# Optimization experiments

Measured on AMD Instinct MI355X. Metric: run time of the kernel, lower is better.

## Reference

```python
import jax, jax.numpy as jnp
import numpy as np

S = 1024; VOCAB = 100000; EMB = 300
POS_SZ = 64; CHAR_E = 50; CHAR_ENC = 128; WLEN = 16
NCHARS = 100; NPOSTAG = 50; NPOSITIONS = 1024
D = EMB + 3 * POS_SZ + CHAR_ENC  # word_rep_size = 620
BIH = 128   # per-direction LSTM hidden (bilstm_hidden_size // 2)
TLH = 256; LCC = 128; GCC = 256
NET = 8; NTAGS = 16; NREL = 16
TOKF = 2 * BIH + LCC + TLH       # 640
SENTF = 2 * TOKF + GCC           # 1536

def _p(k, shape):
    return 0.02 * jax.random.normal(k, shape, dtype=jnp.float32)

def setup_inputs():
    key = jax.random.key(0)
    ks = jax.random.split(key, 30)
    return {
        'word_inputs': jax.random.randint(ks[0], (1, S), 0, VOCAB),
        'char_inputs': jax.random.randint(ks[1], (1, S, WLEN), 0, NCHARS),
        'postag_inputs': jax.random.randint(ks[2], (1, S), 0, NPOSTAG),
        'dependency_inputs': jax.random.randint(ks[3], (1, S), 0, 64),
        'position_inputs': jax.random.randint(ks[4], (1, S), 0, NPOSITIONS),
        'topo_order': jnp.arange(S),  # children-before-parents order
        'parent': jnp.concatenate([jnp.arange(1, S), jnp.array([S])]),  # chain dep tree; root -> dummy slot S
        'pointed_token_idx': 5,
        'word_table': _p(ks[5], (VOCAB, EMB)),
        'char_table': _p(ks[6], (NCHARS, CHAR_E)),
        'char_conv_w': _p(ks[7], (CHAR_ENC, CHAR_E, 3)),
        'char_conv_b': jnp.zeros((CHAR_ENC,), jnp.float32),
        'postag_table': _p(ks[8], (NPOSTAG, POS_SZ)),
        'position_table': _p(ks[9], (NPOSITIONS, POS_SZ)),
        'lstm_f_Wx': _p(ks[10], (D, 4 * BIH)),
        'lstm_f_Wh': _p(ks[11], (BIH, 4 * BIH)),
        'lstm_f_b': jnp.zeros((4 * BIH,), jnp.float32),
        'lstm_b_Wx': _p(ks[12], (D, 4 * BIH)),
        'lstm_b_Wh': _p(ks[13], (BIH, 4 * BIH)),
        'lstm_b_b': jnp.zeros((4 * BIH,), jnp.float32),
        'word_cnn_w': _p(ks[14], (LCC, D, 3)),
        'word_cnn_b': jnp.zeros((LCC,), jnp.float32),
        'tl_Wiou': _p(ks[15], (D, 3 * TLH)),
        'tl_Uiou': _p(ks[16], (TLH, 3 * TLH)),
        'tl_biou': jnp.zeros((3 * TLH,), jnp.float32),
        'tl_Wf': _p(ks[17], (D, TLH)),
        'tl_Uf': _p(ks[18], (TLH, TLH)),
        'tl_bf': jnp.zeros((TLH,), jnp.float32),
        'sent_cnn_w': _p(ks[19], (GCC, D, 3)),
        'sent_cnn_b': jnp.zeros((GCC,), jnp.float32),
        'et_w': _p(ks[20], (GCC + TOKF, NET)),
        'et_b': jnp.zeros((NET,), jnp.float32),
        'crf_w': _p(ks[21], (SENTF, NTAGS)),
        'crf_b': jnp.zeros((NTAGS,), jnp.float32),
        'crf_trans': _p(ks[22], (NTAGS, NTAGS)),
        'rel_w': _p(ks[23], (SENTF, NREL)),
        'rel_b': jnp.zeros((NREL,), jnp.float32),
    }

def _conv1d(x, w, b):
    # x: [N, Cin, W], w: [Cout, Cin, K], padding=1 (matches nn.Conv1d(..., padding=1))
    y = jax.lax.conv_general_dilated(x, w, (1,), [(1, 1)], dimension_numbers=('NCW', 'OIW', 'NCW'))
    return y + b[None, :, None]

def _lstm(xs, Wx, Wh, b):
    H = Wh.shape[0]
    def step(carry, x):
        h, c = carry
        g = x @ Wx + h @ Wh + b
        i, f, gg, o = jnp.split(g, 4, axis=-1)
        c = jax.nn.sigmoid(f) * c + jax.nn.sigmoid(i) * jnp.tanh(gg)
        h = jax.nn.sigmoid(o) * jnp.tanh(c)
        return (h, c), h
    init = (jnp.zeros((H,), xs.dtype), jnp.zeros((H,), xs.dtype))
    _, hs = jax.lax.scan(step, init, xs)
    return hs

def _tree_lstm(x, order, parent, Wiou, Uiou, biou, Wf, Uf, bf):
    # ChildSum TreeLSTM over the whole dependency tree in topological order.
    # Equivalent to the source's per-token subtree recursion: each node's h
    # only depends on its subtree.
    Sn, H = x.shape[0], Uf.shape[0]
    xiou = x @ Wiou + biou                 # [S, 3H]
    xf = jnp.concatenate([x @ Wf + bf, jnp.zeros((1, H), x.dtype)], axis=0)  # dummy row for root's parent
    def step(carry, j):
        h, hsum, fcsum = carry
        iou = xiou[j] + hsum[j] @ Uiou
        i, o, u = jnp.split(iou, 3)
        cj = jax.nn.sigmoid(i) * jnp.tanh(u) + fcsum[j]
        hj = jax.nn.sigmoid(o) * jnp.tanh(cj)
        p = parent[j]
        f = jax.nn.sigmoid(xf[p] + hj @ Uf)  # per-child forget gate
        return (h.at[j].set(hj), hsum.at[p].add(hj), fcsum.at[p].add(f * cj)), None
    h0 = jnp.zeros((Sn, H), x.dtype)
    acc0 = jnp.zeros((Sn + 1, H), x.dtype)
    (h, _, _), _ = jax.lax.scan(step, (h0, acc0, acc0), order)
    return h

def _viterbi(emissions, trans):
    # emissions: [S, T]; trans[i, j] = score(i -> j)
    def step(score, e):
        s = score[:, None] + trans
        return jnp.max(s, axis=0) + e, jnp.argmax(s, axis=0)
    final, ptrs = jax.lax.scan(step, emissions[0], emissions[1:])
    last = jnp.argmax(final)
    def bt(tag, p):
        prev = p[tag]
        return prev, prev
    _, prevs = jax.lax.scan(bt, last, ptrs, reverse=True)
    return jnp.concatenate([prevs, last[None]])

def reference(word_inputs, char_inputs, postag_inputs, dependency_inputs, position_inputs, topo_order, parent, pointed_token_idx, word_table, char_table, char_conv_w, char_conv_b, postag_table, position_table, lstm_f_Wx, lstm_f_Wh, lstm_f_b, lstm_b_Wx, lstm_b_Wh, lstm_b_b, word_cnn_w, word_cnn_b, tl_Wiou, tl_Uiou, tl_biou, tl_Wf, tl_Uf, tl_bf, sent_cnn_w, sent_cnn_b, et_w, et_b, crf_w, crf_b, crf_trans, rel_w, rel_b):
    we = word_table[word_inputs]                                   # [1,S,EMB]
    cx = jnp.transpose(char_table[char_inputs[0]], (0, 2, 1))      # [S,CHAR_E,WLEN]
    ce = jnp.max(jax.nn.relu(_conv1d(cx, char_conv_w, char_conv_b)), axis=-1)[None]  # CharCNN -> [1,S,CHAR_ENC]
    pe = postag_table[postag_inputs]
    poe = position_table[position_inputs]
    de = position_table[dependency_inputs]                         # faithful to source bug: uses position table
    inputs = jnp.concatenate([we, ce, pe, poe, de], axis=-1)       # [1,S,D]
    x = inputs[0]
    hf = _lstm(x, lstm_f_Wx, lstm_f_Wh, lstm_f_b)
    hb = _lstm(x[::-1], lstm_b_Wx, lstm_b_Wh, lstm_b_b)[::-1]
    bilstm = jnp.concatenate([hf, hb], axis=-1)[None]              # [1,S,2*BIH]
    xc = jnp.transpose(inputs, (0, 2, 1))                          # [1,D,S]
    local_cnn = jnp.transpose(_conv1d(xc, word_cnn_w, word_cnn_b), (0, 2, 1))
    tree_h = _tree_lstm(x, topo_order, parent, tl_Wiou, tl_Uiou, tl_biou, tl_Wf, tl_Uf, tl_bf)[None]
    global_cnn = jnp.transpose(jnp.max(_conv1d(xc, sent_cnn_w, sent_cnn_b), axis=-1, keepdims=True), (0, 2, 1))  # [1,1,GCC]
    tokens_info = jnp.concatenate([bilstm, local_cnn, tree_h], axis=-1)  # [1,S,TOKF]
    ptr = tokens_info[:, pointed_token_idx, :]                     # [1,TOKF]
    ptr_info = jnp.broadcast_to(ptr[:, None, :], (1, S, TOKF))
    glob_info = jnp.broadcast_to(global_cnn, (1, S, GCC))
    sentence_encoding = jnp.concatenate([tokens_info, ptr_info, glob_info], axis=-1)  # dropout = identity (eval)
    one_vec = jnp.concatenate([global_cnn[:, 0, :], ptr], axis=-1)
    entitytype = jax.nn.softmax(one_vec @ et_w + et_b, axis=-1)
    entities = _viterbi(sentence_encoding[0] @ crf_w + crf_b, crf_trans)
    relations = jax.nn.sigmoid(sentence_encoding @ rel_w + rel_b)
    return sentence_encoding, entitytype, entities, relations
```

## Files before the change

### kernel.cpp

```cpp
#include <hip/hip_runtime.h>
#include <math.h>

#define SEQ   1024
#define DX    620
#define BIH   128
#define TLH   256
#define NTAGS 16

#define O_X      0
#define O_XGF    634880
#define O_XGB    (O_XGF + 524288)
#define O_XIOU   (O_XGB + 524288)
#define O_XF     (O_XIOU + 786432)
#define O_LCNN   (O_XF + 262400)
#define O_SCNN   (O_LCNN + 131072)
#define O_PART   (O_SCNN + 262144)
#define O_GCNN   (O_PART + 4096)
#define O_HF     (O_GCNN + 256)
#define O_HB     (O_HF + 131072)
#define O_TREEH  (O_HB + 131072)
#define O_IOUA   (O_TREEH + 262144)
#define O_FCSUM  (O_IOUA + 787200)
#define O_EMIS   (O_FCSUM + 262400)
#define O_CNT    (O_EMIS + 16384)

#define SENT 0xFFFFFFFFu

__device__ __forceinline__ float sig_f(float x){ return 1.0f/(1.0f + __expf(-x)); }
__device__ __forceinline__ float tanh_f(float x){
  float ax = fabsf(x);
  float e  = __expf(-2.0f*ax);
  float t  = (1.0f - e)/(1.0f + e);
  return x < 0.0f ? -t : t;
}

__global__ __launch_bounds__(128) void k_embed(
    const int* __restrict__ wi, const int* __restrict__ ci,
    const int* __restrict__ postag_in, const int* __restrict__ dep_in, const int* __restrict__ pos_in,
    const float* __restrict__ word_table, const float* __restrict__ char_table,
    const float* __restrict__ ccw, const float* __restrict__ ccb,
    const float* __restrict__ postag_table, const float* __restrict__ position_table,
    float* __restrict__ x)
{
  int s = blockIdx.x;
  int tid = threadIdx.x;
  __shared__ __align__(16) float ce[50][16];
  for (int idx = tid; idx < 800; idx += 128){
    int e = idx >> 4, t = idx & 15;
    ce[e][t] = char_table[ci[s*16 + t]*50 + e];
  }
  __syncthreads();
  float* xr = x + (size_t)s*DX;
  const float* wrow = word_table + (size_t)wi[s]*300;
  for (int d = tid; d < 300; d += 128) xr[d] = wrow[d];
  {
    int oc = tid;
    const float* wp = ccw + oc*150;
    float acc[16];
    float b = ccb[oc];
    #pragma unroll
    for (int t=0;t<16;t++) acc[t] = b;
    for (int ic=0; ic<50; ic++){
      float w0 = wp[ic*3+0], w1 = wp[ic*3+1], w2 = wp[ic*3+2];
      float cv[16];
      float4 c0 = *(const float4*)&ce[ic][0];
      float4 c1 = *(const float4*)&ce[ic][4];
      float4 c2 = *(const float4*)&ce[ic][8];
      float4 c3 = *(const float4*)&ce[ic][12];
      cv[0]=c0.x;cv[1]=c0.y;cv[2]=c0.z;cv[3]=c0.w;
      cv[4]=c1.x;cv[5]=c1.y;cv[6]=c1.z;cv[7]=c1.w;
      cv[8]=c2.x;cv[9]=c2.y;cv[10]=c2.z;cv[11]=c2.w;
      cv[12]=c3.x;cv[13]=c3.y;cv[14]=c3.z;cv[15]=c3.w;
      #pragma unroll
      for (int t=0;t<16;t++){
        float a = cv[t]*w1;
        if (t > 0)  a += cv[t-1]*w0;
        if (t < 15) a += cv[t+1]*w2;
        acc[t] += a;
      }
    }
    float m = acc[0];
    #pragma unroll
    for (int t=1;t<16;t++) m = fmaxf(m, acc[t]);
    xr[300 + oc] = fmaxf(m, 0.0f);
  }
  if (tid < 64){
    int d = tid;
    xr[428 + d] = postag_table[postag_in[s]*64 + d];
    xr[492 + d] = position_table[pos_in[s]*64 + d];
    xr[556 + d] = position_table[dep_in[s]*64 + d];
  }
}

struct GemmArgs {
  const float* B[6];
  const float* bias[6];
  float*       C[6];
  int N[6]; int K[6]; int amode[6];
};

__global__ __launch_bounds__(256) void k_gemm(const float* __restrict__ x, GemmArgs ga)
{
  int z = blockIdx.z;
  int N = ga.N[z], K = ga.K[z], amode = ga.amode[z];
  int bn = blockIdx.x*64;
  if (bn >= N) return;
  int bm = blockIdx.y*64;
  const float* __restrict__ Bm = ga.B[z];
  __shared__ __align__(16) float As[20][64];
  __shared__ __align__(16) float Bs[20][64];
  int tid = threadIdx.x;
  int lane = tid & 63, kg = tid >> 6;
  int tx = tid & 15, ty = tid >> 4;
  float acc[4][4] = {{0.f}};
  for (int k0 = 0; k0 < K; k0 += 20){
    #pragma unroll
    for (int kk=0; kk<5; kk++){
      int k = kg*5 + kk;
      float av;
      if (amode == 0){
        av = x[(size_t)(bm+lane)*DX + k0 + k];
      } else {
        int kc = k0 + k;
        int d  = kc/3;
        int sh = kc - d*3 - 1;
        int row = bm + lane + sh;
        av = (row >= 0 && row < SEQ) ? x[(size_t)row*DX + d] : 0.0f;
      }
      As[k][lane] = av;
      Bs[k][lane] = (amode==0) ? Bm[(size_t)(k0+k)*N + bn + lane]
                               : Bm[(size_t)(bn+lane)*K + k0 + k];
    }
    __syncthreads();
    #pragma unroll
    for (int k=0;k<20;k++){
      float4 a = *(const float4*)&As[k][ty<<2];
      float4 b = *(const float4*)&Bs[k][tx<<2];
      acc[0][0]+=a.x*b.x; acc[0][1]+=a.x*b.y; acc[0][2]+=a.x*b.z; acc[0][3]+=a.x*b.w;
      acc[1][0]+=a.y*b.x; acc[1][1]+=a.y*b.y; acc[1][2]+=a.y*b.z; acc[1][3]+=a.y*b.w;
      acc[2][0]+=a.z*b.x; acc[2][1]+=a.z*b.y; acc[2][2]+=a.z*b.z; acc[2][3]+=a.z*b.w;
      acc[3][0]+=a.w*b.x; acc[3][1]+=a.w*b.y; acc[3][2]+=a.w*b.z; acc[3][3]+=a.w*b.w;
    }
    __syncthreads();
  }
  const float* bias = ga.bias[z];
  float* C = ga.C[z];
  float4 bb;
  bb.x = bias[bn+(tx<<2)+0]; bb.y = bias[bn+(tx<<2)+1];
  bb.z = bias[bn+(tx<<2)+2]; bb.w = bias[bn+(tx<<2)+3];
  #pragma unroll
  for (int i=0;i<4;i++){
    int row = bm + (ty<<2) + i;
    float4 o;
    o.x = acc[i][0] + bb.x; o.y = acc[i][1] + bb.y;
    o.z = acc[i][2] + bb.z; o.w = acc[i][3] + bb.w;
    *(float4*)&C[(size_t)row*N + bn + (tx<<2)] = o;
  }
}

__global__ __launch_bounds__(256) void k_gmax(const float* __restrict__ scnn, float* __restrict__ gcnn){
  int c = threadIdx.x;
  float m = -3.0e38f;
  #pragma unroll 8
  for (int s = 0; s < SEQ; s++) m = fmaxf(m, scnn[(size_t)s*256 + c]);
  gcnn[c] = m;
}

__global__ __launch_bounds__(1024) void k_recur(
    const float* __restrict__ xg_f, const float* __restrict__ xg_b,
    const float* __restrict__ Wh_f, const float* __restrict__ Wh_b,
    const float* __restrict__ xiou, const float* __restrict__ xf,
    const float* __restrict__ Uiou, const float* __restrict__ Uf,
    const int* __restrict__ order, const int* __restrict__ parent,
    float* __restrict__ hf, float* __restrict__ hb,
    float* tree_h, float* iou_acc, float* fcsum)
{
  int blk = blockIdx.x;
  int tid = threadIdx.x;

  if (blk >= 4){
    const float* xg  = (blk == 4) ? xg_f : xg_b;
    const float* Wh  = (blk == 4) ? Wh_f : Wh_b;
    float* hout      = (blk == 4) ? hf : hb;
    int col = tid & 511, half = tid >> 9;
    float4 w4[16];
    #pragma unroll
    for (int r=0;r<16;r++){
      w4[r].x = Wh[(size_t)(half*64 + r*4+0)*512 + col];
      w4[r].y = Wh[(size_t)(half*64 + r*4+1)*512 + col];
      w4[r].z = Wh[(size_t)(half*64 + r*4+2)*512 + col];
      w4[r].w = Wh[(size_t)(half*64 + r*4+3)*512 + col];
    }
    __shared__ __align__(16) float lhl[BIH];
    __shared__ float lcst[BIH];
    __shared__ float pr[512];
    __shared__ float gl[512];
    if (tid < BIH){ lhl[tid] = 0.f; lcst[tid] = 0.f; }
    __syncthreads();
    for (int st=0; st<SEQ; st++){
      int n = (blk == 4) ? st : (SEQ-1-st);
      float xgv = (half == 0) ? xg[(size_t)n*512 + col] : 0.f;
      float a = 0.f;
      #pragma unroll
      for (int r=0;r<16;r++){
        float4 h4 = *(const float4*)&lhl[half*64 + r*4];
        a += h4.x*w4[r].x + h4.y*w4[r].y + h4.z*w4[r].z + h4.w*w4[r].w;
      }
      if (half) pr[col] = a;
      __syncthreads();
      if (!half) gl[col] = a + pr[col] + xgv;
      __syncthreads();
      if (tid < BIH){
        float gi = gl[tid], gf = gl[BIH+tid], gg = gl[2*BIH+tid], go = gl[3*BIH+tid];
        float c = sig_f(gf)*lcst[tid] + sig_f(gi)*tanh_f(gg);
        float h = sig_f(go)*tanh_f(c);
        lcst[tid] = c;
        lhl[tid] = h;
        hout[(size_t)n*BIH + tid] = h;
      }
      __syncthreads();
    }
    return;
  }

  int q = tid >> 8;
  int c = tid & 255;
  float4 w4[16];
  if (c < 192){
    int gcol = (c>>6)*TLH + blk*64 + (c&63);
    #pragma unroll
    for (int r=0;r<16;r++){
      w4[r].x = Uiou[(size_t)(q*64 + r*4+0)*768 + gcol];
      w4[r].y = Uiou[(size_t)(q*64 + r*4+1)*768 + gcol];
      w4[r].z = Uiou[(size_t)(q*64 + r*4+2)*768 + gcol];
      w4[r].w = Uiou[(size_t)(q*64 + r*4+3)*768 + gcol];
    }
  } else {
    int fcol = blk*64 + (c-192);
    #pragma unroll
    for (int r=0;r<16;r++){
      w4[r].x = Uf[(size_t)(q*64 + r*4+0)*256 + fcol];
      w4[r].y = Uf[(size_t)(q*64 + r*4+1)*256 + fcol];
      w4[r].z = Uf[(size_t)(q*64 + r*4+2)*256 + fcol];
      w4[r].w = Uf[(size_t)(q*64 + r*4+3)*256 + fcol];
    }
  }
  __shared__ __align__(16) float hl[TLH];
  __shared__ float part[256][5];
  __shared__ float cprev[64];
  __shared__ float passv[256];
  __shared__ int ord_l[SEQ];
  __shared__ int par_l[SEQ];
  for (int i=tid; i<SEQ; i+=1024){ ord_l[i] = order[i]; par_l[i] = parent[i]; }
  int ulo = blk*64, uhi = blk*64 + 64;
  __syncthreads();

  for (int t=0; t<SEQ; t++){
    int n = ord_l[t];
    bool ppeq = false;
    float xi=0.f, xo=0.f, xu=0.f;
    if (tid < 64){
      int u = ulo + tid;
      xi = xiou[(size_t)n*768 + u];
      xo = xiou[(size_t)n*768 + 256 + u];
      xu = xiou[(size_t)n*768 + 512 + u];
    }
    if (t > 0){
      int m  = ord_l[t-1];
      int pp = par_l[m];
      ppeq = (pp == n);
      float oldv = 0.f, xfv = 0.f;
      if (tid < 192){
        oldv = iou_acc[(size_t)pp*768 + (tid>>6)*TLH + ulo + (tid&63)];
      } else if (tid < 256){
        int fc = ulo + (tid-192);
        oldv = fcsum[(size_t)pp*256 + fc];
        xfv  = xf[(size_t)pp*256 + fc];
      }
      float a = 0.f;
      #pragma unroll
      for (int r=0;r<16;r++){
        float4 h4 = *(const float4*)&hl[q*64 + r*4];
        a += h4.x*w4[r].x + h4.y*w4[r].y + h4.z*w4[r].z + h4.w*w4[r].w;
      }
      part[c][q] = a;
      __syncthreads();
      if (tid < 256){
        float v = part[tid][0] + part[tid][1] + part[tid][2] + part[tid][3];
        if (tid < 192){
          float tot = oldv + v;
          iou_acc[(size_t)pp*768 + (tid>>6)*TLH + ulo + (tid&63)] = tot;
          passv[tid] = tot;
        } else {
          float fg = sig_f(xfv + v);
          float tot = oldv + fg * cprev[tid-192];
          fcsum[(size_t)pp*256 + ulo + (tid-192)] = tot;
          passv[tid] = tot;
        }
      }
      __syncthreads();
    }
    if (tid < 64){
      int u = ulo + tid;
      float ai, ao, au, fcs;
      if (ppeq){
        ai = passv[tid]; ao = passv[64+tid]; au = passv[128+tid]; fcs = passv[192+tid];
      } else {
        ai = iou_acc[(size_t)n*768 + u];
        ao = iou_acc[(size_t)n*768 + 256 + u];
        au = iou_acc[(size_t)n*768 + 512 + u];
        fcs = fcsum[(size_t)n*256 + u];
      }
      float cc = sig_f(xi + ai)*tanh_f(xu + au) + fcs;
      float hh = sig_f(xo + ao)*tanh_f(cc);
      cprev[tid] = cc;
      hl[u] = hh;
      __hip_atomic_store(&tree_h[(size_t)n*TLH + u], hh, __ATOMIC_RELAXED, __HIP_MEMORY_SCOPE_AGENT);
    }
    if (tid < 256 && (tid < ulo || tid >= uhi)){
      const unsigned* tp = (const unsigned*)(tree_h + (size_t)n*TLH + tid);
      unsigned v = __hip_atomic_load(tp, __ATOMIC_RELAXED, __HIP_MEMORY_SCOPE_AGENT);
      while (v == SENT){
        __builtin_amdgcn_s_sleep(1);
        v = __hip_atomic_load(tp, __ATOMIC_RELAXED, __HIP_MEMORY_SCOPE_AGENT);
      }
      hl[tid] = __uint_as_float(v);
    }
    __syncthreads();
  }
}

__global__ __launch_bounds__(256) void k_assemble(
    const float* __restrict__ hf, const float* __restrict__ hb,
    const float* __restrict__ lcnn, const float* __restrict__ tree_h,
    const float* __restrict__ gcnn,
    const float* __restrict__ crf_w, const float* __restrict__ crf_b,
    const float* __restrict__ rel_w, const float* __restrict__ rel_b,
    const int* __restrict__ ptk,
    float* __restrict__ se_out, float* __restrict__ emis, float* __restrict__ rel_out)
{
  int s = blockIdx.x, tid = threadIdx.x;
  int p = ptk[0];
  __shared__ float se[1536];
  for (int d = tid; d < 1536; d += 256){
    float v;
    if      (d < 128)  v = hf[(size_t)s*128 + d];
    else if (d < 256)  v = hb[(size_t)s*128 + d-128];
    else if (d < 384)  v = lcnn[(size_t)s*128 + d-256];
    else if (d < 640)  v = tree_h[(size_t)s*256 + d-384];
    else if (d < 768)  v = hf[(size_t)p*128 + d-640];
    else if (d < 896)  v = hb[(size_t)p*128 + d-768];
    else if (d < 1024) v = lcnn[(size_t)p*128 + d-896];
    else if (d < 1280) v = tree_h[(size_t)p*256 + d-1024];
    else               v = gcnn[d-1280];
    se[d] = v;
    se_out[(size_t)s*1536 + d] = v;
  }
  __syncthreads();
  int o = tid >> 3, l = tid & 7;
  const float* W = (o < 16) ? crf_w : rel_w;
  int oc = (o < 16) ? o : (o - 16);
  float a = 0.f;
  for (int k = l; k < 1536; k += 8) a += se[k]*W[(size_t)k*16 + oc];
  for (int off = 4; off; off >>= 1) a += __shfl_down(a, off, 8);
  if (l == 0){
    if (o < 16) emis[(size_t)s*16 + o] = a + crf_b[o];
    else        rel_out[(size_t)s*16 + oc] = sig_f(a + rel_b[oc]);
  }
}

__global__ __launch_bounds__(256) void k_entity(
    const float* __restrict__ hf, const float* __restrict__ hb,
    const float* __restrict__ lcnn, const float* __restrict__ tree_h,
    const float* __restrict__ gcnn,
    const float* __restrict__ et_w, const float* __restrict__ et_b,
    const int* __restrict__ ptk, float* __restrict__ out_et)
{
  __shared__ float ov[896];
  __shared__ float lg[8];
  int tid = threadIdx.x;
  int p = ptk[0];
  for (int d = tid; d < 896; d += 256){
    float v;
    if      (d < 256) v = gcnn[d];
    else if (d < 384) v = hf[(size_t)p*128 + d-256];
    else if (d < 512) v = hb[(size_t)p*128 + d-384];
    else if (d < 640) v = lcnn[(size_t)p*128 + d-512];
    else              v = tree_h[(size_t)p*256 + d-640];
    ov[d] = v;
  }
  __syncthreads();
  int o = tid >> 5, l = tid & 31;
  float a = 0.f;
  for (int k = l; k < 896; k += 32) a += ov[k]*et_w[(size_t)k*8 + o];
  for (int off = 16; off; off >>= 1) a += __shfl_down(a, off, 32);
  if (l == 0) lg[o] = a + et_b[o];
  __syncthreads();
  if (tid == 0){
    float mx = lg[0];
    for (int i=1;i<8;i++) mx = fmaxf(mx, lg[i]);
    float e[8], sum = 0.f;
    for (int i=0;i<8;i++){ e[i] = __expf(lg[i]-mx); sum += e[i]; }
    for (int i=0;i<8;i++) out_et[i] = e[i]/sum;
  }
}

__global__ __launch_bounds__(128) void k_viterbi(
    const float* __restrict__ emis, const float* __restrict__ trans, float* __restrict__ out_e)
{
  __shared__ float ring[64][16];
  __shared__ float sc[16], nsc[16];
  __shared__ float tr[256];
  __shared__ unsigned char ptrs[1023*16];
  int tid = threadIdx.x;
  for (int i=tid; i<256; i+=128) tr[i] = trans[i];
  for (int i=tid; i<33*16; i+=128) ring[i>>4][i&15] = emis[i];
  if (tid < 16) sc[tid] = emis[tid];
  __syncthreads();
  int j = (tid & 63) >> 2, iq = tid & 3;
  for (int t=1; t<1024; t++){
    if (tid >= 64){
      int lr = tid - 64;
      int tl = t + 32;
      if (lr < 16 && tl < 1024) ring[tl & 63][lr] = emis[(size_t)tl*16 + lr];
    } else {
      float best = -3.0e38f; int barg = 0;
      #pragma unroll
      for (int ii=0; ii<4; ii++){
        int i = iq*4 + ii;
        float v = sc[i] + tr[i*16 + j];
        if (v > best){ best = v; barg = i; }
      }
      #pragma unroll
      for (int off=1; off<4; off<<=1){
        float ovv = __shfl_down(best, off, 4);
        int   oaa = __shfl_down(barg, off, 4);
        if (ovv > best){ best = ovv; barg = oaa; }
      }
      if (iq == 0){
        nsc[j] = best + ring[t & 63][j];
        ptrs[(t-1)*16 + j] = (unsigned char)barg;
      }
    }
    __syncthreads();
    if (tid < 16) sc[tid] = nsc[tid];
    __syncthreads();
  }
  if (tid == 0){
    float b = sc[0]; int last = 0;
    #pragma unroll
    for (int i=1;i<16;i++){ if (sc[i] > b){ b = sc[i]; last = i; } }
    out_e[1023] = (float)last;
    int cur = last;
    for (int t=1022; t>=0; t--){ cur = (int)ptrs[t*16 + cur]; out_e[t] = (float)cur; }
  }
}

extern "C" void kernel_launch(void* const* d_in, const int* in_sizes, int n_in,
                              void* d_out, int out_size, void* d_ws, size_t ws_size,
                              hipStream_t stream)
{
  (void)in_sizes; (void)n_in; (void)out_size; (void)ws_size;
  const int*   wi         = (const int*)d_in[0];
  const int*   ci         = (const int*)d_in[1];
  const int*   postag_in  = (const int*)d_in[2];
  const int*   dep_in     = (const int*)d_in[3];
  const int*   pos_in     = (const int*)d_in[4];
  const int*   order      = (const int*)d_in[5];
  const int*   parent     = (const int*)d_in[6];
  const int*   ptk        = (const int*)d_in[7];
  const float* word_table = (const float*)d_in[8];
  const float* char_table = (const float*)d_in[9];
  const float* ccw        = (const float*)d_in[10];
  const float* ccb        = (const float*)d_in[11];
  const float* postag_tab = (const float*)d_in[12];
  const float* pos_tab    = (const float*)d_in[13];
  const float* Wx_f       = (const float*)d_in[14];
  const float* Wh_f       = (const float*)d_in[15];
  const float* b_f        = (const float*)d_in[16];
  const float* Wx_b       = (const float*)d_in[17];
  const float* Wh_b       = (const float*)d_in[18];
  const float* b_b        = (const float*)d_in[19];
  const float* wcnn_w     = (const float*)d_in[20];
  const float* wcnn_b     = (const float*)d_in[21];
  const float* Wiou       = (const float*)d_in[22];
  const float* Uiou       = (const float*)d_in[23];
  const float* biou       = (const float*)d_in[24];
  const float* Wf_t       = (const float*)d_in[25];
  const float* Uf_t       = (const float*)d_in[26];
  const float* bf_t       = (const float*)d_in[27];
  const float* scnn_w     = (const float*)d_in[28];
  const float* scnn_b     = (const float*)d_in[29];
  const float* et_w       = (const float*)d_in[30];
  const float* et_b       = (const float*)d_in[31];
  const float* crf_w      = (const float*)d_in[32];
  const float* crf_b      = (const float*)d_in[33];
  const float* crf_trans  = (const float*)d_in[34];
  const float* rel_w      = (const float*)d_in[35];
  const float* rel_b      = (const float*)d_in[36];

  float* ws = (float*)d_ws;
  float* x      = ws + O_X;
  float* xg_f   = ws + O_XGF;
  float* xg_b   = ws + O_XGB;
  float* xiou   = ws + O_XIOU;
  float* xf     = ws + O_XF;
  float* lcnn   = ws + O_LCNN;
  float* scnn   = ws + O_SCNN;
  float* gcnn   = ws + O_GCNN;
  float* hf     = ws + O_HF;
  float* hb     = ws + O_HB;
  float* tree_h = ws + O_TREEH;
  float* iou_acc= ws + O_IOUA;
  float* fcsum  = ws + O_FCSUM;
  float* emis   = ws + O_EMIS;

  float* outF     = (float*)d_out;
  float* se_out   = outF;
  float* et_out   = outF + 1572864;
  float* ent_out  = outF + 1572872;
  float* rel_out  = outF + 1573896;

  hipMemsetAsync(xf, 0, (size_t)1025*256*sizeof(float), stream);
  hipMemsetAsync(iou_acc, 0, ((size_t)1025*768 + 1025*256)*sizeof(float), stream);
  hipMemsetAsync(tree_h, 0xFF, (size_t)1024*256*sizeof(float), stream);

  k_embed<<<SEQ, 128, 0, stream>>>(wi, ci, postag_in, dep_in, pos_in,
                                   word_table, char_table, ccw, ccb,
                                   postag_tab, pos_tab, x);

  GemmArgs ga;
  ga.B[0]=Wx_f;  ga.bias[0]=b_f;   ga.C[0]=xg_f; ga.N[0]=512; ga.K[0]=620;  ga.amode[0]=0;
  ga.B[1]=Wx_b;  ga.bias[1]=b_b;   ga.C[1]=xg_b; ga.N[1]=512; ga.K[1]=620;  ga.amode[1]=0;
  ga.B[2]=Wiou;  ga.bias[2]=biou;  ga.C[2]=xiou; ga.N[2]=768; ga.K[2]=620;  ga.amode[2]=0;
  ga.B[3]=Wf_t;  ga.bias[3]=bf_t;  ga.C[3]=xf;   ga.N[3]=256; ga.K[3]=620;  ga.amode[3]=0;
  ga.B[4]=wcnn_w;ga.bias[4]=wcnn_b;ga.C[4]=lcnn; ga.N[4]=128; ga.K[4]=1860; ga.amode[4]=1;
  ga.B[5]=scnn_w;ga.bias[5]=scnn_b;ga.C[5]=scnn; ga.N[5]=256; ga.K[5]=1860; ga.amode[5]=1;
  k_gemm<<<dim3(12,16,6), 256, 0, stream>>>(x, ga);

  k_gmax<<<1, 256, 0, stream>>>(scnn, gcnn);

  k_recur<<<6, 1024, 0, stream>>>(xg_f, xg_b, Wh_f, Wh_b, xiou, xf, Uiou, Uf_t,
                                  order, parent, hf, hb, tree_h, iou_acc, fcsum);

  k_assemble<<<SEQ, 256, 0, stream>>>(hf, hb, lcnn, tree_h, gcnn,
                                      crf_w, crf_b, rel_w, rel_b, ptk,
                                      se_out, emis, rel_out);

  k_entity<<<1, 256, 0, stream>>>(hf, hb, lcnn, tree_h, gcnn, et_w, et_b, ptk, et_out);

  k_viterbi<<<1, 128, 0, stream>>>(emis, crf_trans, ent_out);
}
```

Before: 2.912 ms.

## Shrink recurrent blocks to 512 threads and cut per-step barriers

The recurrent kernel now runs 512 threads per block, each holding 128 weight rows in registers. The BiLSTM drops the two-half split, its shared partial-sum buffer and one barrier per step. The tree-LSTM splits each column across a thread pair, reduces with a lane shuffle, and moves the global loads of accumulator and parent state ahead of the matvec, which removes one barrier per step. Cross-block hidden-state polling now uses 48 threads reading four values each, without sleeping. In exchange, register pressure per thread roughly doubles, and the busy-wait spin without sleep may add memory contention.

```diff
diff --git a/kernel.cpp b/kernel.cpp
--- a/kernel.cpp
+++ b/kernel.cpp
@@ -22,7 +22,6 @@
 #define O_IOUA   (O_TREEH + 262144)
 #define O_FCSUM  (O_IOUA + 787200)
 #define O_EMIS   (O_FCSUM + 262400)
-#define O_CNT    (O_EMIS + 16384)
 
 #define SENT 0xFFFFFFFFu
 
@@ -166,7 +165,7 @@
   gcnn[c] = m;
 }
 
-__global__ __launch_bounds__(1024) void k_recur(
+__global__ __launch_bounds__(512, 2) void k_recur(
     const float* __restrict__ xg_f, const float* __restrict__ xg_b,
     const float* __restrict__ Wh_f, const float* __restrict__ Wh_b,
     const float* __restrict__ xiou, const float* __restrict__ xf,
@@ -182,33 +181,33 @@
     const float* xg  = (blk == 4) ? xg_f : xg_b;
     const float* Wh  = (blk == 4) ? Wh_f : Wh_b;
     float* hout      = (blk == 4) ? hf : hb;
-    int col = tid & 511, half = tid >> 9;
-    float4 w4[16];
-    #pragma unroll
-    for (int r=0;r<16;r++){
-      w4[r].x = Wh[(size_t)(half*64 + r*4+0)*512 + col];
-      w4[r].y = Wh[(size_t)(half*64 + r*4+1)*512 + col];
-      w4[r].z = Wh[(size_t)(half*64 + r*4+2)*512 + col];
-      w4[r].w = Wh[(size_t)(half*64 + r*4+3)*512 + col];
-    }
+    int col = tid;
+    float4 w4[32];
+    #pragma unroll
+    for (int r=0;r<32;r++){
+      w4[r].x = Wh[(size_t)(r*4+0)*512 + col];
+      w4[r].y = Wh[(size_t)(r*4+1)*512 + col];
+      w4[r].z = Wh[(size_t)(r*4+2)*512 + col];
+      w4[r].w = Wh[(size_t)(r*4+3)*512 + col];
+    }
+    #pragma unroll
+    for (int r=0;r<32;r++)
+      asm volatile("" : "+v"(w4[r].x), "+v"(w4[r].y), "+v"(w4[r].z), "+v"(w4[r].w));
     __shared__ __align__(16) float lhl[BIH];
     __shared__ float lcst[BIH];
-    __shared__ float pr[512];
     __shared__ float gl[512];
     if (tid < BIH){ lhl[tid] = 0.f; lcst[tid] = 0.f; }
     __syncthreads();
+    const float4* lhl4 = (const float4*)lhl;
     for (int st=0; st<SEQ; st++){
       int n = (blk == 4) ? st : (SEQ-1-st);
-      float xgv = (half == 0) ? xg[(size_t)n*512 + col] : 0.f;
-      float a = 0.f;
+      float a = xg[(size_t)n*512 + col];
       #pragma unroll
-      for (int r=0;r<16;r++){
-        float4 h4 = *(const float4*)&lhl[half*64 + r*4];
+      for (int r=0;r<32;r++){
+        float4 h4 = lhl4[r];
         a += h4.x*w4[r].x + h4.y*w4[r].y + h4.z*w4[r].z + h4.w*w4[r].w;
       }
-      if (half) pr[col] = a;
-      __syncthreads();
-      if (!half) gl[col] = a + pr[col] + xgv;
+      gl[col] = a;
       __syncthreads();
       if (tid < BIH){
         float gi = gl[tid], gf = gl[BIH+tid], gg = gl[2*BIH+tid], go = gl[3*BIH+tid];
@@ -223,108 +222,112 @@
     return;
   }
 
-  int q = tid >> 8;
-  int c = tid & 255;
-  float4 w4[16];
-  if (c < 192){
-    int gcol = (c>>6)*TLH + blk*64 + (c&63);
-    #pragma unroll
-    for (int r=0;r<16;r++){
-      w4[r].x = Uiou[(size_t)(q*64 + r*4+0)*768 + gcol];
-      w4[r].y = Uiou[(size_t)(q*64 + r*4+1)*768 + gcol];
-      w4[r].z = Uiou[(size_t)(q*64 + r*4+2)*768 + gcol];
-      w4[r].w = Uiou[(size_t)(q*64 + r*4+3)*768 + gcol];
-    }
-  } else {
-    int fcol = blk*64 + (c-192);
-    #pragma unroll
-    for (int r=0;r<16;r++){
-      w4[r].x = Uf[(size_t)(q*64 + r*4+0)*256 + fcol];
-      w4[r].y = Uf[(size_t)(q*64 + r*4+1)*256 + fcol];
-      w4[r].z = Uf[(size_t)(q*64 + r*4+2)*256 + fcol];
-      w4[r].w = Uf[(size_t)(q*64 + r*4+3)*256 + fcol];
-    }
-  }
+  int colh = tid >> 1, half = tid & 1;
+  int ulo = blk*64;
+  float4 w4[32];
+  {
+    const float* Wsrc; size_t stride; int gcol;
+    if (colh < 192){ Wsrc = Uiou; stride = 768; gcol = (colh>>6)*TLH + ulo + (colh&63); }
+    else           { Wsrc = Uf;   stride = 256; gcol = ulo + (colh-192); }
+    #pragma unroll
+    for (int r=0;r<32;r++){
+      int row = half*128 + r*4;
+      w4[r].x = Wsrc[(size_t)(row+0)*stride + gcol];
+      w4[r].y = Wsrc[(size_t)(row+1)*stride + gcol];
+      w4[r].z = Wsrc[(size_t)(row+2)*stride + gcol];
+      w4[r].w = Wsrc[(size_t)(row+3)*stride + gcol];
+    }
+  }
+  #pragma unroll
+  for (int r=0;r<32;r++)
+    asm volatile("" : "+v"(w4[r].x), "+v"(w4[r].y), "+v"(w4[r].z), "+v"(w4[r].w));
+
   __shared__ __align__(16) float hl[TLH];
-  __shared__ float part[256][5];
+  __shared__ float colsum[TLH];
   __shared__ float cprev[64];
-  __shared__ float passv[256];
   __shared__ int ord_l[SEQ];
   __shared__ int par_l[SEQ];
-  for (int i=tid; i<SEQ; i+=1024){ ord_l[i] = order[i]; par_l[i] = parent[i]; }
-  int ulo = blk*64, uhi = blk*64 + 64;
+  for (int i=tid; i<SEQ; i+=512){ ord_l[i] = order[i]; par_l[i] = parent[i]; }
   __syncthreads();
+  const float4* hl4 = (const float4*)hl;
 
   for (int t=0; t<SEQ; t++){
-    int n = ord_l[t];
-    bool ppeq = false;
-    float xi=0.f, xo=0.f, xu=0.f;
+    int n  = ord_l[t];
+    int m  = (t > 0) ? ord_l[t-1] : 0;
+    int pp = (t > 0) ? par_l[m] : -1;
+    bool ppeq = (pp == n);
+
+    float xi=0.f, xo=0.f, xu=0.f, ac_i=0.f, ac_o=0.f, ac_u=0.f, fcn=0.f;
+    float xfv=0.f, po_i=0.f, po_o=0.f, po_u=0.f, po_f=0.f;
     if (tid < 64){
-      int u = ulo + tid;
-      xi = xiou[(size_t)n*768 + u];
-      xo = xiou[(size_t)n*768 + 256 + u];
-      xu = xiou[(size_t)n*768 + 512 + u];
-    }
+      int uu = ulo + tid;
+      xi   = xiou[(size_t)n*768 + uu];
+      xo   = xiou[(size_t)n*768 + 256 + uu];
+      xu   = xiou[(size_t)n*768 + 512 + uu];
+      ac_i = iou_acc[(size_t)n*768 + uu];
+      ac_o = iou_acc[(size_t)n*768 + 256 + uu];
+      ac_u = iou_acc[(size_t)n*768 + 512 + uu];
+      fcn  = fcsum[(size_t)n*256 + uu];
+      if (t > 0){
+        xfv = xf[(size_t)pp*256 + uu];
+        if (!ppeq){
+          po_i = iou_acc[(size_t)pp*768 + uu];
+          po_o = iou_acc[(size_t)pp*768 + 256 + uu];
+          po_u = iou_acc[(size_t)pp*768 + 512 + uu];
+          po_f = fcsum[(size_t)pp*256 + uu];
+        }
+      }
+    }
+
     if (t > 0){
-      int m  = ord_l[t-1];
-      int pp = par_l[m];
-      ppeq = (pp == n);
-      float oldv = 0.f, xfv = 0.f;
-      if (tid < 192){
-        oldv = iou_acc[(size_t)pp*768 + (tid>>6)*TLH + ulo + (tid&63)];
-      } else if (tid < 256){
-        int fc = ulo + (tid-192);
-        oldv = fcsum[(size_t)pp*256 + fc];
-        xfv  = xf[(size_t)pp*256 + fc];
-      }
       float a = 0.f;
       #pragma unroll
-      for (int r=0;r<16;r++){
-        float4 h4 = *(const float4*)&hl[q*64 + r*4];
+      for (int r=0;r<32;r++){
+        float4 h4 = hl4[half*32 + r];
         a += h4.x*w4[r].x + h4.y*w4[r].y + h4.z*w4[r].z + h4.w*w4[r].w;
       }
-      part[c][q] = a;
-      __syncthreads();
-      if (tid < 256){
-        float v = part[tid][0] + part[tid][1] + part[tid][2] + part[tid][3];
-        if (tid < 192){
-          float tot = oldv + v;
-          iou_acc[(size_t)pp*768 + (tid>>6)*TLH + ulo + (tid&63)] = tot;
-          passv[tid] = tot;
+      a += __shfl_xor(a, 1);
+      if (!half) colsum[colh] = a;
+    }
+    __syncthreads();
+
+    if (tid < 64){
+      int uu = ulo + tid;
+      float ai = ac_i, ao = ac_o, au = ac_u, fcs = fcn;
+      if (t > 0){
+        float vi = colsum[tid], vo = colsum[64+tid], vuu = colsum[128+tid], vf = colsum[192+tid];
+        float fg  = sig_f(xfv + vf);
+        float fcc = fg * cprev[tid];
+        if (ppeq){
+          ai += vi; ao += vo; au += vuu; fcs += fcc;
         } else {
-          float fg = sig_f(xfv + v);
-          float tot = oldv + fg * cprev[tid-192];
-          fcsum[(size_t)pp*256 + ulo + (tid-192)] = tot;
-          passv[tid] = tot;
+          iou_acc[(size_t)pp*768 + uu]       = po_i + vi;
+          iou_acc[(size_t)pp*768 + 256 + uu] = po_o + vo;
+          iou_acc[(size_t)pp*768 + 512 + uu] = po_u + vuu;
+          fcsum[(size_t)pp*256 + uu]         = po_f + fcc;
         }
-      }
-      __syncthreads();
-    }
-    if (tid < 64){
-      int u = ulo + tid;
-      float ai, ao, au, fcs;
-      if (ppeq){
-        ai = passv[tid]; ao = passv[64+tid]; au = passv[128+tid]; fcs = passv[192+tid];
-      } else {
-        ai = iou_acc[(size_t)n*768 + u];
-        ao = iou_acc[(size_t)n*768 + 256 + u];
-        au = iou_acc[(size_t)n*768 + 512 + u];
-        fcs = fcsum[(size_t)n*256 + u];
       }
       float cc = sig_f(xi + ai)*tanh_f(xu + au) + fcs;
       float hh = sig_f(xo + ao)*tanh_f(cc);
       cprev[tid] = cc;
-      hl[u] = hh;
-      __hip_atomic_store(&tree_h[(size_t)n*TLH + u], hh, __ATOMIC_RELAXED, __HIP_MEMORY_SCOPE_AGENT);
-    }
-    if (tid < 256 && (tid < ulo || tid >= uhi)){
-      const unsigned* tp = (const unsigned*)(tree_h + (size_t)n*TLH + tid);
-      unsigned v = __hip_atomic_load(tp, __ATOMIC_RELAXED, __HIP_MEMORY_SCOPE_AGENT);
-      while (v == SENT){
-        __builtin_amdgcn_s_sleep(1);
-        v = __hip_atomic_load(tp, __ATOMIC_RELAXED, __HIP_MEMORY_SCOPE_AGENT);
-      }
-      hl[tid] = __uint_as_float(v);
+      hl[uu] = hh;
+      __hip_atomic_store(&tree_h[(size_t)n*TLH + uu], hh, __ATOMIC_RELAXED, __HIP_MEMORY_SCOPE_AGENT);
+    } else if (tid >= 64 && tid < 112){
+      int p  = tid - 64;
+      int qi = (p < (ulo >> 2)) ? p : p + 16;
+      const unsigned* tp = (const unsigned*)(tree_h + (size_t)n*TLH + qi*4);
+      unsigned v0, v1, v2, v3;
+      while (true){
+        v0 = __hip_atomic_load(tp+0, __ATOMIC_RELAXED, __HIP_MEMORY_SCOPE_AGENT);
+        v1 = __hip_atomic_load(tp+1, __ATOMIC_RELAXED, __HIP_MEMORY_SCOPE_AGENT);
+        v2 = __hip_atomic_load(tp+2, __ATOMIC_RELAXED, __HIP_MEMORY_SCOPE_AGENT);
+        v3 = __hip_atomic_load(tp+3, __ATOMIC_RELAXED, __HIP_MEMORY_SCOPE_AGENT);
+        if ((v0 != SENT) & (v1 != SENT) & (v2 != SENT) & (v3 != SENT)) break;
+      }
+      float4 hv;
+      hv.x = __uint_as_float(v0); hv.y = __uint_as_float(v1);
+      hv.z = __uint_as_float(v2); hv.w = __uint_as_float(v3);
+      *(float4*)&hl[qi*4] = hv;
     }
     __syncthreads();
   }
@@ -540,8 +543,8 @@
 
   k_gmax<<<1, 256, 0, stream>>>(scnn, gcnn);
 
-  k_recur<<<6, 1024, 0, stream>>>(xg_f, xg_b, Wh_f, Wh_b, xiou, xf, Uiou, Uf_t,
-                                  order, parent, hf, hb, tree_h, iou_acc, fcsum);
+  k_recur<<<6, 512, 0, stream>>>(xg_f, xg_b, Wh_f, Wh_b, xiou, xf, Uiou, Uf_t,
+                                 order, parent, hf, hb, tree_h, iou_acc, fcsum);
 
   k_assemble<<<SEQ, 256, 0, stream>>>(hf, hb, lcnn, tree_h, gcnn,
                                       crf_w, crf_b, rel_w, rel_b, ptk,
```

New measurement: 3.084 ms. 1.06x slower.
